# Performance work log

Hardware: AMD Instinct MI355X
Metric: run time of the kernel (lower is better)

Reference implementation:

```python
import jax, jax.numpy as jnp
import numpy as np

N_PTS = 65534      # 2**16 - 2 from rand_subset
N_VARS = 24        # len(mesh.full_varlist); cols 0/1/2 = lat_deg/lon_deg/reltime_hours
RES = 1.0          # config.latent_res (degrees)
GH, GW = 180, 360  # len(latent_lats), len(latent_lons)
CL = 512           # config.latent_size
TR_DIM, TR_TOK, DEPTH, HEADS, DH = 128, 4, 2, 8, 16
PE_NUM = 8         # DEFAULT_POSEMB_NUM
DA_HALF = 12.0     # mesh.da_window_size / 2
EMB_IN = N_VARS + 3 * (1 + 2 * PE_NUM)  # 75


def setup_inputs() -> dict:
    key = jax.random.key(0)
    ks = jax.random.split(key, 12)
    feats = jax.random.normal(ks[0], (N_PTS, N_VARS), dtype=jnp.float32) * 0.5
    lat = jax.random.uniform(ks[1], (N_PTS,), minval=-90.0, maxval=90.0)
    lon = jax.random.uniform(ks[2], (N_PTS,), minval=-180.0, maxval=180.0)
    t = jax.random.uniform(ks[3], (N_PTS,), minval=-12.0, maxval=12.0)
    x = feats.at[:, 0].set(lat).at[:, 1].set(lon).at[:, 2].set(t)
    w = lambda k, s: jax.random.normal(k, s, dtype=jnp.float32) * 0.02
    return dict(
        x=x,
        W_emb=w(ks[4], (EMB_IN, TR_DIM * TR_TOK)), b_emb=jnp.zeros(TR_DIM * TR_TOK),
        ln1_s=jnp.ones((DEPTH, TR_DIM)), ln1_b=jnp.zeros((DEPTH, TR_DIM)),
        Wqkv=w(ks[5], (DEPTH, TR_DIM, 3 * TR_DIM)), bqkv=jnp.zeros((DEPTH, 3 * TR_DIM)),
        Wo=w(ks[6], (DEPTH, TR_DIM, TR_DIM)), bo=jnp.zeros((DEPTH, TR_DIM)),
        ln2_s=jnp.ones((DEPTH, TR_DIM)), ln2_b=jnp.zeros((DEPTH, TR_DIM)),
        Wf1=w(ks[7], (DEPTH, TR_DIM, 4 * TR_DIM)), bf1=jnp.zeros((DEPTH, 4 * TR_DIM)),
        Wf2=w(ks[8], (DEPTH, 4 * TR_DIM, TR_DIM)), bf2=jnp.zeros((DEPTH, TR_DIM)),
        W_comb=w(ks[9], (TR_DIM * TR_TOK, CL)), b_comb=jnp.zeros(CL),
    )


def _ln(h, s, b):
    m = jnp.mean(h, -1, keepdims=True)
    v = jnp.var(h, -1, keepdims=True)
    return (h - m) * jax.lax.rsqrt(v + 1e-5) * s + b


def _posemb(p):  # p: [N,3] -> [N, 3*(1+2*PE_NUM)]
    freqs = 2.0 ** jnp.arange(PE_NUM, dtype=p.dtype)
    ang = p[..., None] * freqs * jnp.pi  # [N,3,PE_NUM]
    n = p.shape[0]
    return jnp.concatenate([p, jnp.sin(ang).reshape(n, -1), jnp.cos(ang).reshape(n, -1)], axis=1)


def reference(x, W_emb, b_emb, ln1_s, ln1_b, Wqkv, bqkv, Wo, bo,
              ln2_s, ln2_b, Wf1, bf1, Wf2, bf2, W_comb, b_comb):
    lat = x[:, 0]
    lat = jnp.where(lat == -90.0, lat + 1e-4, lat)
    lon = x[:, 1]
    t = x[:, 2]
    # lat/lon -> latent grid indices
    lati = jnp.floor((90.0 - lat) / RES).astype(jnp.int32)
    loni = jnp.mod(180.0 / RES + jnp.floor((lon + 180.0) / RES), 360.0 / RES).astype(jnp.int32)
    # fractional cell position + relative time for sinusoidal posemb
    lat_th = jnp.mod(-lat, RES) / RES
    lon_th = jnp.mod(lon, RES) / RES
    t_th = t + 1.0
    pe = _posemb(jnp.stack([lat_th, lon_th, t_th], axis=-1))
    xn = x.at[:, 0].set(lat / 90.0).at[:, 1].set(lon / 180.0).at[:, 2].set(t / DA_HALF)
    feat = jnp.concatenate([xn, pe], axis=1)  # [N, 75]
    h = (feat @ W_emb + b_emb).reshape(-1, TR_TOK, TR_DIM)  # [N, 4, 128]
    for i in range(DEPTH):  # pre-norm transformer blocks
        a = _ln(h, ln1_s[i], ln1_b[i])
        qkv = (a @ Wqkv[i] + bqkv[i]).reshape(-1, TR_TOK, 3, HEADS, DH)
        q, k, v = qkv[:, :, 0], qkv[:, :, 1], qkv[:, :, 2]  # [N,T,H,D]
        att = jnp.einsum('nqhd,nkhd->nhqk', q, k) / np.sqrt(DH).astype(np.float32)
        att = jax.nn.softmax(att, axis=-1)
        o = jnp.einsum('nhqk,nkhd->nqhd', att, v).reshape(-1, TR_TOK, TR_DIM)
        h = h + (o @ Wo[i] + bo[i])
        f = _ln(h, ln2_s[i], ln2_b[i])
        h = h + jax.nn.gelu(f @ Wf1[i] + bf1[i]) @ Wf2[i] + bf2[i]
    y = h.reshape(-1, TR_TOK * TR_DIM) @ W_comb + b_comb  # [N, CL]
    flat = lati * GW + loni  # [N] segment ids into H*W grid
    sums = jax.ops.segment_sum(y, flat, num_segments=GH * GW)
    cnt = jax.ops.segment_sum(jnp.ones((y.shape[0],), y.dtype), flat, num_segments=GH * GW)
    reduced = sums / jnp.clip(cnt, 1.0)[:, None]  # scatter_mean semantics (empty cells -> 0)
    return reduced.reshape(1, 1, GH, GW, CL)
```

## Files before the change

### kernel.cpp

```cpp
#include <hip/hip_runtime.h>
#include <hip/hip_bf16.h>
#include <math.h>

#define N_PTS 65534
#define GH 180
#define GW 360
#define NCELL (GH*GW)
#define PI_F 3.14159265358979323846f
#define NSEC 92

typedef __bf16 bf16;
typedef bf16 bf16x8 __attribute__((ext_vector_type(8)));
typedef float f32x4 __attribute__((ext_vector_type(4)));

#define LDS_FENCE() asm volatile("s_waitcnt lgkmcnt(0)" ::: "memory")
#define RAW_BAR()   asm volatile("s_barrier" ::: "memory")

static __device__ __forceinline__ f32x4 mfma16(bf16x8 a, bf16x8 b, f32x4 c){
    return __builtin_amdgcn_mfma_f32_16x16x32_bf16(a,b,c,0,0,0);
}

__global__ void repack_kernel(const float* __restrict__ W_emb,
                              const float* __restrict__ Wqkv,
                              const float* __restrict__ Wo,
                              const float* __restrict__ Wf1,
                              const float* __restrict__ Wf2,
                              const float* __restrict__ W_comb,
                              bf16* __restrict__ stream){
    int idx = blockIdx.x*256 + threadIdx.x;
    if (idx >= NSEC*8192) return;
    int sec = idx >> 13;
    int r   = idx & 8191;
    int u   = r >> 9;
    int e   = r & 511;
    int l   = e >> 3, j = e & 7;
    int g   = l >> 4, c = l & 15;
    float v = 0.f;
    if (sec < 8){
        if (u < 12){
            int nt=u/3, ks=u%3;
            int n = sec*64 + nt*16 + c;
            int k = ks*32 + g*8 + j;
            if (k < 75) v = W_emb[(size_t)k*512 + n];
        }
    } else if (sec < 60){
        int lay = (sec-8)/26, s = (sec-8)%26;
        if (s < 8){
            if (u < 12){
                int s3=u/4, ks=u%4;
                int col = s3*128 + s*16 + c;
                int k = ks*32 + g*8 + j;
                v = Wqkv[(size_t)lay*49152 + (size_t)k*384 + col];
            }
        } else if (s < 10){
            int nh = (s-8)*4 + u/4, ks = u%4;
            int k = ks*32 + g*8 + j;
            v = Wo[(size_t)lay*16384 + (size_t)k*128 + nh*16 + c];
        } else {
            int t = s-10, ch = t>>1;
            if (!(t&1)){
                int nt=u/4, ks=u%4;
                int n = ch*64 + nt*16 + c;
                int k = ks*32 + g*8 + j;
                v = Wf1[(size_t)lay*65536 + (size_t)k*512 + n];
            } else {
                int nt2=u/2, ks=u%2;
                int kk = ks*32 + g*8 + j;
                v = Wf2[(size_t)lay*65536 + (size_t)(ch*64+kk)*128 + nt2*16 + c];
            }
        }
    } else {
        int chk = sec-60, tk=u/4, ks=u%4;
        int n = chk*16 + c;
        int k = tk*128 + ks*32 + g*8 + j;
        v = W_comb[(size_t)k*512 + n];
    }
    stream[idx] = (bf16)v;
}

__global__ void count_kernel(const float* __restrict__ x, int* __restrict__ flat,
                             int* __restrict__ cnt){
    int p = blockIdx.x*256 + threadIdx.x;
    if (p >= N_PTS) return;
    float lat = x[p*24+0], lon = x[p*24+1];
    if (lat == -90.0f) lat += 1e-4f;
    int lati = (int)floorf(90.0f - lat);
    int loni = (180 + (int)floorf(lon + 180.0f)) % 360;
    lati = min(max(lati,0),GH-1);
    loni = min(max(loni,0),GW-1);
    int f = lati*GW + loni;
    flat[p] = f;
    atomicAdd(&cnt[f], 1);
}

#define ADV() do{ \
    { int4* wb4 = (int4*)&wbuf[sec&1][0]; \
      wb4[tid]=p0; wb4[tid+256]=p1; wb4[tid+512]=p2; wb4[tid+768]=p3; } \
    if (sec+1 < NSEC){ const int4* gp = gs4 + (size_t)(sec+1)*1024; \
      p0=gp[tid]; p1=gp[tid+256]; p2=gp[tid+512]; p3=gp[tid+768]; } \
    LDS_FENCE(); RAW_BAR(); \
    cb = &wbuf[sec&1][0]; sec++; \
}while(0)

#define FRAG(u) (*(const bf16x8*)&cb[(u)*512 + l8])

#define P_EMB  0
#define P_QKV  512
#define P_O    1280
#define P_F1   1536
#define P_F2   2560
#define P_L1S  2816
#define P_L1B  3072
#define P_L2S  3328
#define P_L2B  3584
#define P_CMB  3840

__global__ __launch_bounds__(256,2) void fused_kernel(
    const float* __restrict__ x,
    const bf16* __restrict__ stream,
    const float* __restrict__ b_emb, const float* __restrict__ bqkv,
    const float* __restrict__ bo,    const float* __restrict__ bf1,
    const float* __restrict__ bf2,   const float* __restrict__ b_comb,
    const float* __restrict__ ln1s,  const float* __restrict__ ln1b,
    const float* __restrict__ ln2s,  const float* __restrict__ ln2b,
    const int* __restrict__ flat,    const int* __restrict__ cnt,
    float* __restrict__ out)
{
    __shared__ __align__(16) bf16  tile[4][32][136];
    __shared__ __align__(16) bf16  wbuf[2][8192];
    __shared__ __align__(16) bf16  prm[4352];
    const int tid = threadIdx.x;
    const int wv = tid>>6, l = tid&63;
    const int g = l>>4, c = l&15;
    const int l8 = l*8;
    const int pb = blockIdx.x*32 + wv*8;

    const int4* gs4 = (const int4*)stream;
    int4 p0,p1,p2,p3;
    p0=gs4[tid]; p1=gs4[tid+256]; p2=gs4[tid+512]; p3=gs4[tid+768];

    for (int i=tid; i<4352; i+=256){
        float v;
        if      (i<512)  v=b_emb[i];
        else if (i<1280) v=bqkv[i-512];
        else if (i<1536) v=bo[i-1280];
        else if (i<2560) v=bf1[i-1536];
        else if (i<2816) v=bf2[i-2560];
        else if (i<3072) v=ln1s[i-2816];
        else if (i<3328) v=ln1b[i-3072];
        else if (i<3584) v=ln2s[i-3328];
        else if (i<3840) v=ln2b[i-3584];
        else             v=b_comb[i-3840];
        prm[i]=(bf16)v;
    }

    int flj[4]; float ivj[4];
    #pragma unroll
    for (int j=0;j<4;++j){
        int p = pb + g*4 + j;
        if (g<2 && p<N_PTS){ int f=flat[p]; flj[j]=f;
            ivj[j]=__builtin_amdgcn_rcpf(fmaxf((float)cnt[f],1.f)); }
        else { flj[j]=0; ivj[j]=0.f; }
    }

    {
        const int pl = l>>3, w = l&7;
        const int p = pb + pl;
        const bool valid = (p < N_PTS);
        const int row  = (pl<4)? (pl*4)   : ((pl-4)*4+1);
        const int zrow = (pl<4)? (pl*4+2) : ((pl-4)*4+3);
        float lat=0.f, lon=0.f, t=0.f;
        if (valid){ lat=x[p*24+0]; lon=x[p*24+1]; t=x[p*24+2]; }
        if (lat == -90.0f) lat += 1e-4f;
        float pvs[3] = { -lat - floorf(-lat), lon - floorf(lon), t + 1.0f };
        #pragma unroll
        for (int i=0;i<12;++i){
            int f = w*12 + i;
            float val;
            if (f >= 75) val = 0.f;
            else if (f < 24){
                if (f==0)      val = lat*(1.f/90.f);
                else if (f==1) val = lon*(1.f/180.f);
                else if (f==2) val = t*(1.f/12.f);
                else           val = valid ? x[p*24+f] : 0.f;
            } else if (f<27) val = pvs[f-24];
            else if (f<51){ int q=f-27; val = sinf(pvs[q>>3]*(float)(1<<(q&7))*PI_F); }
            else          { int q=f-51; val = cosf(pvs[q>>3]*(float)(1<<(q&7))*PI_F); }
            if (!valid) val = 0.f;
            tile[wv][row][f]  = (bf16)val;
            tile[wv][zrow][f] = (bf16)0.f;
        }
    }
    LDS_FENCE();
    bf16x8 afe[3];
    #pragma unroll
    for (int ks=0;ks<3;++ks) afe[ks] = *(const bf16x8*)&tile[wv][c][ks*32+g*8];

    int sec = 0;
    const bf16* cb = &wbuf[0][0];

    f32x4 h[2][8];
    #pragma unroll
    for (int ch=0; ch<8; ++ch){
        ADV();
        const int tk = ch>>1;
        const int hn = (ch&1)*4;
        #pragma unroll
        for (int nt=0; nt<4; ++nt){
            f32x4 acc = {0.f,0.f,0.f,0.f};
            #pragma unroll
            for (int ks=0;ks<3;++ks)
                acc = mfma16(afe[ks], FRAG(nt*3+ks), acc);
            float bb = (float)prm[P_EMB + ch*64 + nt*16 + c];
            h[0][hn+nt][tk] = acc[0] + bb;
            h[1][hn+nt][tk] = acc[1] + bb;
        }
    }

    for (int lay=0; lay<2; ++lay){
        float ls[8], lb[8];
        #pragma unroll
        for (int n=0;n<8;++n){ ls[n]=(float)prm[P_L1S+lay*128+n*16+c]; lb[n]=(float)prm[P_L1B+lay*128+n*16+c]; }
        #pragma unroll
        for (int mt=0;mt<2;++mt)
            #pragma unroll
            for (int j=0;j<4;++j){
                float s=0.f,q=0.f;
                #pragma unroll
                for (int n=0;n<8;++n){ float v=h[mt][n][j]; s+=v; q+=v*v; }
                s += __shfl_xor(s,1); s += __shfl_xor(s,2); s += __shfl_xor(s,4); s += __shfl_xor(s,8);
                q += __shfl_xor(q,1); q += __shfl_xor(q,2); q += __shfl_xor(q,4); q += __shfl_xor(q,8);
                float m = s*(1.f/128.f);
                float var = q*(1.f/128.f) - m*m;
                float rs = rsqrtf(var + 1e-5f);
                #pragma unroll
                for (int n=0;n<8;++n)
                    tile[wv][mt*16+g*4+j][n*16+c] = (bf16)((h[mt][n][j]-m)*rs*ls[n]+lb[n]);
            }
        LDS_FENCE();
        bf16x8 af[2][4];
        #pragma unroll
        for (int mt=0;mt<2;++mt)
            #pragma unroll
            for (int ks=0;ks<4;++ks)
                af[mt][ks] = *(const bf16x8*)&tile[wv][mt*16+c][ks*32+g*8];
        LDS_FENCE();
        for (int hd=0; hd<8; ++hd){
            ADV();
            f32x4 acc[3][2];
            #pragma unroll
            for (int s3=0;s3<3;++s3){
                bf16x8 bq[4];
                #pragma unroll
                for (int ks=0;ks<4;++ks) bq[ks] = FRAG(s3*4+ks);
                float bias = (float)prm[P_QKV + lay*384 + s3*128 + hd*16 + c];
                #pragma unroll
                for (int mt=0;mt<2;++mt){
                    f32x4 a = {0.f,0.f,0.f,0.f};
                    #pragma unroll
                    for (int ks=0;ks<4;++ks)
                        a = mfma16(af[mt][ks], bq[ks], a);
                    #pragma unroll
                    for (int j=0;j<4;++j) a[j] += bias;
                    acc[s3][mt] = a;
                }
            }
            #pragma unroll
            for (int mt=0;mt<2;++mt){
                #pragma unroll
                for (int j=0;j<4;++j) acc[0][mt][j] *= 0.36067376f;
                float att[16];
                #pragma unroll
                for (int i=0;i<4;++i)
                    #pragma unroll
                    for (int j=0;j<4;++j){
                        float t = acc[0][mt][i]*acc[1][mt][j];
                        t += __shfl_xor(t,1); t += __shfl_xor(t,2);
                        t += __shfl_xor(t,4); t += __shfl_xor(t,8);
                        att[i*4+j]=t;
                    }
                #pragma unroll
                for (int i=0;i<4;++i){
                    float m = fmaxf(fmaxf(att[i*4],att[i*4+1]),fmaxf(att[i*4+2],att[i*4+3]));
                    float e0=exp2f(att[i*4]-m),   e1=exp2f(att[i*4+1]-m);
                    float e2=exp2f(att[i*4+2]-m), e3=exp2f(att[i*4+3]-m);
                    float inv = __builtin_amdgcn_rcpf(e0+e1+e2+e3);
                    float o = (e0*acc[2][mt][0]+e1*acc[2][mt][1]+e2*acc[2][mt][2]+e3*acc[2][mt][3])*inv;
                    tile[wv][mt*16+g*4+i][hd*16+c] = (bf16)o;
                }
            }
        }
        LDS_FENCE();
        bf16x8 oa[2][4];
        #pragma unroll
        for (int mt=0;mt<2;++mt)
            #pragma unroll
            for (int ks=0;ks<4;++ks)
                oa[mt][ks] = *(const bf16x8*)&tile[wv][mt*16+c][ks*32+g*8];
        LDS_FENCE();
        for (int s2=0; s2<2; ++s2){
            ADV();
            #pragma unroll
            for (int n4=0;n4<4;++n4){
                int nh = s2*4+n4;
                bf16x8 bo_[4];
                #pragma unroll
                for (int ks=0;ks<4;++ks) bo_[ks] = FRAG(n4*4+ks);
                float bias = (float)prm[P_O + lay*128 + nh*16 + c];
                #pragma unroll
                for (int mt=0;mt<2;++mt){
                    f32x4 a = h[mt][nh];
                    #pragma unroll
                    for (int ks=0;ks<4;++ks)
                        a = mfma16(oa[mt][ks], bo_[ks], a);
                    #pragma unroll
                    for (int j=0;j<4;++j) a[j]+=bias;
                    h[mt][nh]=a;
                }
            }
        }
        #pragma unroll
        for (int n=0;n<8;++n){ ls[n]=(float)prm[P_L2S+lay*128+n*16+c]; lb[n]=(float)prm[P_L2B+lay*128+n*16+c]; }
        #pragma unroll
        for (int mt=0;mt<2;++mt)
            #pragma unroll
            for (int j=0;j<4;++j){
                float s=0.f,q=0.f;
                #pragma unroll
                for (int n=0;n<8;++n){ float v=h[mt][n][j]; s+=v; q+=v*v; }
                s += __shfl_xor(s,1); s += __shfl_xor(s,2); s += __shfl_xor(s,4); s += __shfl_xor(s,8);
                q += __shfl_xor(q,1); q += __shfl_xor(q,2); q += __shfl_xor(q,4); q += __shfl_xor(q,8);
                float m = s*(1.f/128.f);
                float var = q*(1.f/128.f) - m*m;
                float rs = rsqrtf(var + 1e-5f);
                #pragma unroll
                for (int n=0;n<8;++n)
                    tile[wv][mt*16+g*4+j][n*16+c] = (bf16)((h[mt][n][j]-m)*rs*ls[n]+lb[n]);
            }
        LDS_FENCE();
        bf16x8 f1a[2][4];
        #pragma unroll
        for (int mt=0;mt<2;++mt)
            #pragma unroll
            for (int ks=0;ks<4;++ks)
                f1a[mt][ks] = *(const bf16x8*)&tile[wv][mt*16+c][ks*32+g*8];
        LDS_FENCE();
        for (int ch=0; ch<8; ++ch){
            ADV();
            #pragma unroll
            for (int nt=0;nt<4;++nt){
                bf16x8 b1[4];
                #pragma unroll
                for (int ks=0;ks<4;++ks) b1[ks] = FRAG(nt*4+ks);
                float bias = (float)prm[P_F1 + lay*512 + ch*64 + nt*16 + c];
                #pragma unroll
                for (int mt=0;mt<2;++mt){
                    f32x4 a = {0.f,0.f,0.f,0.f};
                    #pragma unroll
                    for (int ks=0;ks<4;++ks)
                        a = mfma16(f1a[mt][ks], b1[ks], a);
                    #pragma unroll
                    for (int j=0;j<4;++j){
                        float xx = a[j]+bias;
                        float t2 = xx*xx;
                        float pp = fmaf(t2, 0.044715f, 1.0f);
                        float w2 = xx*pp;
                        float u  = exp2f(-2.3022082f*w2);
                        float r  = __builtin_amdgcn_rcpf(1.0f+u);
                        tile[wv][mt*16+g*4+j][nt*16+c] = (bf16)(xx*r);
                    }
                }
            }
            LDS_FENCE();
            bf16x8 ga[2][2];
            #pragma unroll
            for (int mt=0;mt<2;++mt)
                #pragma unroll
                for (int ks=0;ks<2;++ks)
                    ga[mt][ks] = *(const bf16x8*)&tile[wv][mt*16+c][ks*32+g*8];
            LDS_FENCE();
            ADV();
            #pragma unroll
            for (int nt2=0;nt2<8;++nt2){
                bf16x8 b2[2];
                #pragma unroll
                for (int ks=0;ks<2;++ks) b2[ks] = FRAG(nt2*2+ks);
                #pragma unroll
                for (int mt=0;mt<2;++mt){
                    f32x4 a = h[mt][nt2];
                    #pragma unroll
                    for (int ks=0;ks<2;++ks)
                        a = mfma16(ga[mt][ks], b2[ks], a);
                    h[mt][nt2]=a;
                }
            }
        }
        #pragma unroll
        for (int nt2=0;nt2<8;++nt2){
            float bias = (float)prm[P_F2 + lay*128 + nt2*16+c];
            #pragma unroll
            for (int mt=0;mt<2;++mt)
                #pragma unroll
                for (int j=0;j<4;++j) h[mt][nt2][j]+=bias;
        }
    }

    #pragma unroll
    for (int mt=0;mt<2;++mt)
        #pragma unroll
        for (int n=0;n<8;++n)
            #pragma unroll
            for (int j=0;j<4;++j)
                tile[wv][mt*16+g*4+j][n*16+c] = (bf16)h[mt][n][j];
    LDS_FENCE();
    bf16x8 afc[4][4];
    #pragma unroll
    for (int tk=0;tk<4;++tk)
        #pragma unroll
        for (int ks=0;ks<4;++ks)
            afc[tk][ks] = *(const bf16x8*)&tile[wv][(c&7)*4+tk][ks*32+g*8];
    for (int chk=0; chk<32; ++chk){
        ADV();
        f32x4 a = {0.f,0.f,0.f,0.f};
        #pragma unroll
        for (int tk=0;tk<4;++tk)
            #pragma unroll
            for (int ks=0;ks<4;++ks)
                a = mfma16(afc[tk][ks], FRAG(tk*4+ks), a);
        if (g<2){
            float bb = (float)prm[P_CMB + chk*16+c];
            #pragma unroll
            for (int j=0;j<4;++j){
                int p = pb + g*4 + j;
                if (p < N_PTS)
                    atomicAdd(&out[(size_t)flj[j]*512 + chk*16 + c], (a[j]+bb)*ivj[j]);
            }
        }
    }
}

extern "C" void kernel_launch(void* const* d_in, const int* in_sizes, int n_in,
                              void* d_out, int out_size, void* d_ws, size_t ws_size,
                              hipStream_t stream){
    (void)in_sizes; (void)n_in; (void)ws_size;
    const float* x      = (const float*)d_in[0];
    const float* W_emb  = (const float*)d_in[1];
    const float* b_emb  = (const float*)d_in[2];
    const float* ln1_s  = (const float*)d_in[3];
    const float* ln1_b  = (const float*)d_in[4];
    const float* Wqkv   = (const float*)d_in[5];
    const float* bqkv   = (const float*)d_in[6];
    const float* Wo     = (const float*)d_in[7];
    const float* bo     = (const float*)d_in[8];
    const float* ln2_s  = (const float*)d_in[9];
    const float* ln2_b  = (const float*)d_in[10];
    const float* Wf1    = (const float*)d_in[11];
    const float* bf1    = (const float*)d_in[12];
    const float* Wf2    = (const float*)d_in[13];
    const float* bf2    = (const float*)d_in[14];
    const float* W_comb = (const float*)d_in[15];
    const float* b_comb = (const float*)d_in[16];
    float* out = (float*)d_out;

    char* ws = (char*)d_ws;
    size_t off = 0;
    auto alloc = [&](size_t bytes)->char*{
        char* p = ws + off; off = (off + bytes + 255) & ~(size_t)255; return p;
    };
    bf16* wstream = (bf16*) alloc((size_t)NSEC*8192*2);
    int*  flat    = (int*)  alloc((size_t)N_PTS*4);
    int*  cnt     = (int*)  alloc((size_t)NCELL*4);

    hipMemsetAsync(d_out, 0, (size_t)out_size*sizeof(float), stream);
    hipMemsetAsync(cnt, 0, (size_t)NCELL*4, stream);

    repack_kernel<<<(NSEC*8192+255)/256, 256, 0, stream>>>(
        W_emb, Wqkv, Wo, Wf1, Wf2, W_comb, wstream);
    count_kernel<<<(N_PTS+255)/256, 256, 0, stream>>>(x, flat, cnt);

    fused_kernel<<<2048, 256, 0, stream>>>(x, wstream,
        b_emb, bqkv, bo, bf1, bf2, b_comb,
        ln1_s, ln1_b, ln2_s, ln2_b, flat, cnt, out);
}
```

Baseline: 841.1 us.

## Read weight fragments directly from global memory instead of staging in LDS

Removes the double-buffered LDS weight staging, along with its per-section barriers and register prefetch. Each wave now loads its MFMA B fragments straight from the pre-packed bf16 stream in global memory, relying on L1/L2 caching. This frees 32KB of LDS, and the launch bounds are raised to 3 blocks per CU for higher occupancy. The cost is more global and cache traffic per wave with no software prefetch, so load latency may be exposed before each MFMA.

```diff
diff --git a/kernel.cpp b/kernel.cpp
--- a/kernel.cpp
+++ b/kernel.cpp
@@ -14,7 +14,6 @@
 typedef float f32x4 __attribute__((ext_vector_type(4)));
 
 #define LDS_FENCE() asm volatile("s_waitcnt lgkmcnt(0)" ::: "memory")
-#define RAW_BAR()   asm volatile("s_barrier" ::: "memory")
 
 static __device__ __forceinline__ f32x4 mfma16(bf16x8 a, bf16x8 b, f32x4 c){
     return __builtin_amdgcn_mfma_f32_16x16x32_bf16(a,b,c,0,0,0);
@@ -93,16 +92,7 @@
     atomicAdd(&cnt[f], 1);
 }
 
-#define ADV() do{ \
-    { int4* wb4 = (int4*)&wbuf[sec&1][0]; \
-      wb4[tid]=p0; wb4[tid+256]=p1; wb4[tid+512]=p2; wb4[tid+768]=p3; } \
-    if (sec+1 < NSEC){ const int4* gp = gs4 + (size_t)(sec+1)*1024; \
-      p0=gp[tid]; p1=gp[tid+256]; p2=gp[tid+512]; p3=gp[tid+768]; } \
-    LDS_FENCE(); RAW_BAR(); \
-    cb = &wbuf[sec&1][0]; sec++; \
-}while(0)
-
-#define FRAG(u) (*(const bf16x8*)&cb[(u)*512 + l8])
+#define GFRAG(sb,u) ((sb)[(u)*64 + l])
 
 #define P_EMB  0
 #define P_QKV  512
@@ -115,7 +105,7 @@
 #define P_L2B  3584
 #define P_CMB  3840
 
-__global__ __launch_bounds__(256,2) void fused_kernel(
+__global__ __launch_bounds__(256,3) void fused_kernel(
     const float* __restrict__ x,
     const bf16* __restrict__ stream,
     const float* __restrict__ b_emb, const float* __restrict__ bqkv,
@@ -127,17 +117,12 @@
     float* __restrict__ out)
 {
     __shared__ __align__(16) bf16  tile[4][32][136];
-    __shared__ __align__(16) bf16  wbuf[2][8192];
     __shared__ __align__(16) bf16  prm[4352];
     const int tid = threadIdx.x;
     const int wv = tid>>6, l = tid&63;
     const int g = l>>4, c = l&15;
-    const int l8 = l*8;
     const int pb = blockIdx.x*32 + wv*8;
-
-    const int4* gs4 = (const int4*)stream;
-    int4 p0,p1,p2,p3;
-    p0=gs4[tid]; p1=gs4[tid+256]; p2=gs4[tid+512]; p3=gs4[tid+768];
+    const bf16x8* gs8 = (const bf16x8*)stream;
 
     for (int i=tid; i<4352; i+=256){
         float v;
@@ -162,6 +147,8 @@
             ivj[j]=__builtin_amdgcn_rcpf(fmaxf((float)cnt[f],1.f)); }
         else { flj[j]=0; ivj[j]=0.f; }
     }
+
+    __syncthreads();
 
     {
         const int pl = l>>3, w = l&7;
@@ -196,13 +183,10 @@
     #pragma unroll
     for (int ks=0;ks<3;++ks) afe[ks] = *(const bf16x8*)&tile[wv][c][ks*32+g*8];
 
-    int sec = 0;
-    const bf16* cb = &wbuf[0][0];
-
     f32x4 h[2][8];
     #pragma unroll
     for (int ch=0; ch<8; ++ch){
-        ADV();
+        const bf16x8* sb = gs8 + (size_t)ch*1024;
         const int tk = ch>>1;
         const int hn = (ch&1)*4;
         #pragma unroll
@@ -210,7 +194,7 @@
             f32x4 acc = {0.f,0.f,0.f,0.f};
             #pragma unroll
             for (int ks=0;ks<3;++ks)
-                acc = mfma16(afe[ks], FRAG(nt*3+ks), acc);
+                acc = mfma16(afe[ks], GFRAG(sb, nt*3+ks), acc);
             float bb = (float)prm[P_EMB + ch*64 + nt*16 + c];
             h[0][hn+nt][tk] = acc[0] + bb;
             h[1][hn+nt][tk] = acc[1] + bb;
@@ -246,13 +230,13 @@
                 af[mt][ks] = *(const bf16x8*)&tile[wv][mt*16+c][ks*32+g*8];
         LDS_FENCE();
         for (int hd=0; hd<8; ++hd){
-            ADV();
+            const bf16x8* sb = gs8 + (size_t)(8 + lay*26 + hd)*1024;
             f32x4 acc[3][2];
             #pragma unroll
             for (int s3=0;s3<3;++s3){
                 bf16x8 bq[4];
                 #pragma unroll
-                for (int ks=0;ks<4;++ks) bq[ks] = FRAG(s3*4+ks);
+                for (int ks=0;ks<4;++ks) bq[ks] = GFRAG(sb, s3*4+ks);
                 float bias = (float)prm[P_QKV + lay*384 + s3*128 + hd*16 + c];
                 #pragma unroll
                 for (int mt=0;mt<2;++mt){
@@ -299,13 +283,13 @@
                 oa[mt][ks] = *(const bf16x8*)&tile[wv][mt*16+c][ks*32+g*8];
         LDS_FENCE();
         for (int s2=0; s2<2; ++s2){
-            ADV();
+            const bf16x8* sb = gs8 + (size_t)(8 + lay*26 + 8 + s2)*1024;
             #pragma unroll
             for (int n4=0;n4<4;++n4){
                 int nh = s2*4+n4;
                 bf16x8 bo_[4];
                 #pragma unroll
-                for (int ks=0;ks<4;++ks) bo_[ks] = FRAG(n4*4+ks);
+                for (int ks=0;ks<4;++ks) bo_[ks] = GFRAG(sb, n4*4+ks);
                 float bias = (float)prm[P_O + lay*128 + nh*16 + c];
                 #pragma unroll
                 for (int mt=0;mt<2;++mt){
@@ -346,12 +330,13 @@
                 f1a[mt][ks] = *(const bf16x8*)&tile[wv][mt*16+c][ks*32+g*8];
         LDS_FENCE();
         for (int ch=0; ch<8; ++ch){
-            ADV();
+            const bf16x8* sb1 = gs8 + (size_t)(8 + lay*26 + 10 + ch*2)*1024;
+            const bf16x8* sb2 = sb1 + 1024;
             #pragma unroll
             for (int nt=0;nt<4;++nt){
                 bf16x8 b1[4];
                 #pragma unroll
-                for (int ks=0;ks<4;++ks) b1[ks] = FRAG(nt*4+ks);
+                for (int ks=0;ks<4;++ks) b1[ks] = GFRAG(sb1, nt*4+ks);
                 float bias = (float)prm[P_F1 + lay*512 + ch*64 + nt*16 + c];
                 #pragma unroll
                 for (int mt=0;mt<2;++mt){
@@ -379,12 +364,11 @@
                 for (int ks=0;ks<2;++ks)
                     ga[mt][ks] = *(const bf16x8*)&tile[wv][mt*16+c][ks*32+g*8];
             LDS_FENCE();
-            ADV();
             #pragma unroll
             for (int nt2=0;nt2<8;++nt2){
                 bf16x8 b2[2];
                 #pragma unroll
-                for (int ks=0;ks<2;++ks) b2[ks] = FRAG(nt2*2+ks);
+                for (int ks=0;ks<2;++ks) b2[ks] = GFRAG(sb2, nt2*2+ks);
                 #pragma unroll
                 for (int mt=0;mt<2;++mt){
                     f32x4 a = h[mt][nt2];
@@ -420,13 +404,13 @@
         for (int ks=0;ks<4;++ks)
             afc[tk][ks] = *(const bf16x8*)&tile[wv][(c&7)*4+tk][ks*32+g*8];
     for (int chk=0; chk<32; ++chk){
-        ADV();
+        const bf16x8* sb = gs8 + (size_t)(60 + chk)*1024;
         f32x4 a = {0.f,0.f,0.f,0.f};
         #pragma unroll
         for (int tk=0;tk<4;++tk)
             #pragma unroll
             for (int ks=0;ks<4;++ks)
-                a = mfma16(afc[tk][ks], FRAG(tk*4+ks), a);
+                a = mfma16(afc[tk][ks], GFRAG(sb, tk*4+ks), a);
         if (g<2){
             float bb = (float)prm[P_CMB + chk*16+c];
             #pragma unroll
```

Result: slower. 939.3 us (+11.7%).
